# Kernel optimization log

Measured on AMD Instinct MI355X. Metric: run time of the kernel, lower is better.

Reference implementation:

```python
import jax, jax.numpy as jnp
import numpy as np

DISCOUNT = 0.997
LAMBDA = 0.95
LOSS_SCALE = 0.5
NUM_BINS = 255
BIN_LO, BIN_HI = -20.0, 20.0


def setup_inputs() -> dict:
    key = jax.random.key(0)
    k0, k1, k2, k3 = jax.random.split(key, 4)
    B, H, D = 1024, 16, 4096
    latents = jax.random.normal(k0, (B, H, D), dtype=jnp.float32)
    rewards = jax.random.normal(k1, (B, H), dtype=jnp.float32)
    dones = jnp.zeros((B, H), dtype=jnp.float32)
    bootstrap_latent = jax.random.normal(k2, (B, D), dtype=jnp.float32)
    W = jax.random.normal(k3, (D, NUM_BINS), dtype=jnp.float32) * (1.0 / np.sqrt(D))
    b = jnp.zeros((NUM_BINS,), dtype=jnp.float32)
    return {"latents": latents, "rewards": rewards, "dones": dones,
            "bootstrap_latent": bootstrap_latent, "W": W, "b": b}


def _bin_centers():
    return jnp.linspace(BIN_LO, BIN_HI, NUM_BINS, dtype=jnp.float32)


def _value_head(x, W, b):
    # x: (N, D) -> logits (N, K), value (N,)
    logits = x @ W + b
    value = jax.nn.softmax(logits, axis=-1) @ _bin_centers()
    return value, logits


def _target_to_bins(returns_flat):
    # two-hot encoding onto uniform bins; returns (N, K) soft target
    step = (BIN_HI - BIN_LO) / (NUM_BINS - 1)
    pos = (jnp.clip(returns_flat, BIN_LO, BIN_HI) - BIN_LO) / step  # in [0, K-1]
    low = jnp.clip(jnp.floor(pos).astype(jnp.int32), 0, NUM_BINS - 2)
    frac = pos - low.astype(pos.dtype)
    oh_lo = jax.nn.one_hot(low, NUM_BINS, dtype=returns_flat.dtype)
    oh_hi = jax.nn.one_hot(low + 1, NUM_BINS, dtype=returns_flat.dtype)
    return (1.0 - frac)[:, None] * oh_lo + frac[:, None] * oh_hi


def _lambda_returns(rewards, values, dones, bootstrap_value):
    # backward linear recurrence: G_t = r_t + gamma*mask_t*((1-lam)*V_{t+1} + lam*G_{t+1})
    next_values = jnp.concatenate([values[:, 1:], bootstrap_value[:, None]], axis=1)
    xs = (rewards.T, next_values.T, (1.0 - dones).T)  # time-major (H, B)

    def step(carry, x):
        r, nv, m = x
        g = r + DISCOUNT * m * ((1.0 - LAMBDA) * nv + LAMBDA * carry)
        return g, g

    _, outs = jax.lax.scan(step, bootstrap_value, xs, reverse=True)
    return outs.T  # (B, H)


def reference(latents, rewards, dones, bootstrap_latent, W, b):
    B, H = rewards.shape
    flat_latents = latents.reshape(-1, latents.shape[-1])  # (B*H, D)
    values_flat, logits = _value_head(flat_latents, W, b)
    values = values_flat.reshape(B, H)

    bootstrap_value, _ = _value_head(bootstrap_latent, W, b)
    bootstrap_value = jax.lax.stop_gradient(bootstrap_value)

    returns = jax.lax.stop_gradient(
        _lambda_returns(rewards, jax.lax.stop_gradient(values), dones, bootstrap_value))

    target = _target_to_bins(returns.reshape(-1))  # (B*H, K)
    logp = jax.nn.log_softmax(logits, axis=-1)
    value_loss = jnp.mean(-jnp.sum(target * logp, axis=-1))
    total_loss = LOSS_SCALE * value_loss

    return jnp.stack([total_loss, value_loss, values.mean(), returns.mean(),
                      jnp.std(values, ddof=1), jnp.std(returns, ddof=1)])
```

## Files before the change

kernel.cpp:

```cpp
#include <hip/hip_runtime.h>
#include <math.h>

#define NBINS 255
#define BIN_LO_F (-20.0f)
#define BIN_HI_F (20.0f)

typedef __attribute__((ext_vector_type(8))) short short8;
typedef __attribute__((ext_vector_type(16))) float f32x16;

__device__ __forceinline__ unsigned short f2bf(float f) {
    unsigned u = __builtin_bit_cast(unsigned, f);
    unsigned r = u + 0x7fffu + ((u >> 16) & 1u);
    return (unsigned short)(r >> 16);
}

__device__ __forceinline__ unsigned pkbf(float lo, float hi) {
    unsigned d;
    asm("v_cvt_pk_bf16_f32 %0, %1, %2" : "=v"(d) : "v"(lo), "v"(hi));
    return d;
}

__device__ __forceinline__ short8 mk8(unsigned a, unsigned b, unsigned c, unsigned d) {
    union { unsigned u[4]; short8 s; } t;
    t.u[0] = a; t.u[1] = b; t.u[2] = c; t.u[3] = d;
    return t.s;
}

__device__ __forceinline__ void glds16(const void* g, void* l) {
    __builtin_amdgcn_global_load_lds(
        (const __attribute__((address_space(1))) unsigned int*)g,
        (__attribute__((address_space(3))) unsigned int*)l, 16, 0, 0);
}

__device__ __forceinline__ double wave_reduce_sum_d(double v) {
    #pragma unroll
    for (int m = 32; m >= 1; m >>= 1) v += __shfl_xor(v, m, 64);
    return v;
}

__global__ __launch_bounds__(256) void pack_w4(
    const float* __restrict__ W, char* __restrict__ WpackB)
{
    int u = blockIdx.x * 256 + threadIdx.x;
    int kt = u >> 10;
    int v  = u & 1023;
    int ks = v >> 9;
    int lh = (v >> 8) & 1;
    int gcol = (v >> 5) & 7;
    int c31  = v & 31;
    int col  = gcol * 32 + c31;
    int k0   = kt * 32 + ks * 16 + lh * 8;
    short8 s;
    #pragma unroll
    for (int e = 0; e < 8; ++e)
        s[e] = (col < NBINS) ? (short)f2bf(W[(size_t)(k0 + e) * NBINS + col]) : (short)0;
    *(short8*)(WpackB + (size_t)u * 16) = s;
}

__global__ __launch_bounds__(256, 4) void gemm_mfma_v9(
    const float* __restrict__ latents, const float* __restrict__ boot,
    const char* __restrict__ WpackB, const float* __restrict__ bvec,
    float* __restrict__ logits, int NR, int R, int D, int nwg8)
{
    __shared__ __align__(16) char ldsA[2][4096];
    __shared__ __align__(16) char ldsB[2][16384];

    const int tid  = threadIdx.x;
    const int wave = tid >> 6, lane = tid & 63;
    const int l31  = lane & 31, lhi = lane >> 5;
    const int NT   = D >> 5;

    int bid  = blockIdx.x;
    int work = (bid & 7) * nwg8 + (bid >> 3);
    const int row0 = work * 32;

    const int arow_loc = (wave << 3) + (lane >> 3);
    const int arow = row0 + arow_loc;
    const float* arowp = (arow < NR) ? latents + (size_t)arow * D
                                     : boot + (size_t)(arow - NR) * D;
    const float* asrc = arowp + (((lane & 7) ^ (arow_loc & 7)) << 2);

    const int abase = l31 << 7;
    const int axor  = l31 & 7;

    f32x16 acc0, acc1;
    #pragma unroll
    for (int r = 0; r < 16; ++r) { acc0[r] = 0.f; acc1[r] = 0.f; }

#define STAGE(T, BUF) do {                                                  \
        glds16(asrc + (size_t)(T) * 32, &ldsA[BUF][(wave << 10) + (lane << 4)]); \
        const char* bs_ = WpackB + (size_t)(T) * 16384 + (wave << 12) + (lane << 4); \
        char* bd_ = &ldsB[BUF][(wave << 12) + (lane << 4)];                 \
        glds16(bs_,        bd_);                                            \
        glds16(bs_ + 1024, bd_ + 1024);                                     \
        glds16(bs_ + 2048, bd_ + 2048);                                     \
        glds16(bs_ + 3072, bd_ + 3072);                                     \
    } while (0)

#define COMPUTE(BUF) do {                                                   \
        const char* ab_ = &ldsA[BUF][0];                                    \
        const char* bb_ = &ldsB[BUF][0] + (wave << 10) + (l31 << 4);        \
        _Pragma("unroll")                                                   \
        for (int ks = 0; ks < 2; ++ks) {                                    \
            int c0_ = ks * 4 + lhi * 2;                                     \
            float4 f0_ = *(const float4*)(ab_ + abase + (((c0_ + 0) ^ axor) << 4)); \
            float4 f1_ = *(const float4*)(ab_ + abase + (((c0_ + 1) ^ axor) << 4)); \
            short8 a_  = mk8(pkbf(f0_.x, f0_.y), pkbf(f0_.z, f0_.w),        \
                             pkbf(f1_.x, f1_.y), pkbf(f1_.z, f1_.w));       \
            short8 b0_ = *(const short8*)(bb_ + ((ks * 2 + lhi) << 12));    \
            short8 b1_ = *(const short8*)(bb_ + ((ks * 2 + lhi) << 12) + 512); \
            acc0 = __builtin_amdgcn_mfma_f32_32x32x16_bf16(a_, b0_, acc0, 0, 0, 0); \
            acc1 = __builtin_amdgcn_mfma_f32_32x32x16_bf16(a_, b1_, acc1, 0, 0, 0); \
        }                                                                   \
    } while (0)

#define BAR()   __builtin_amdgcn_s_barrier()
#define SCHED() __builtin_amdgcn_sched_barrier(0)
#define WAITV5() asm volatile("s_waitcnt vmcnt(5)" ::: "memory")
#define WAITV0() asm volatile("s_waitcnt vmcnt(0)" ::: "memory")

    STAGE(0, 0);

    int t = 0;
    for (; t + 3 < NT; t += 2) {
        BAR(); SCHED(); STAGE(t + 1, 1); SCHED(); WAITV5(); BAR(); SCHED(); COMPUTE(0);
        BAR(); SCHED(); STAGE(t + 2, 0); SCHED(); WAITV5(); BAR(); SCHED(); COMPUTE(1);
    }
    BAR(); SCHED(); STAGE(NT - 1, 1); SCHED(); WAITV5(); BAR(); SCHED(); COMPUTE(0);
    BAR(); SCHED(); WAITV0(); BAR(); SCHED(); COMPUTE(1);

#undef STAGE
#undef COMPUTE
#undef BAR
#undef SCHED
#undef WAITV5
#undef WAITV0

    #pragma unroll
    for (int i = 0; i < 2; ++i) {
        int col = wave * 64 + i * 32 + l31;
        if (col < NBINS) {
            float bias = bvec[col];
            const f32x16& a = i ? acc1 : acc0;
            #pragma unroll
            for (int r = 0; r < 16; ++r) {
                int row = row0 + (r & 3) + 8 * (r >> 2) + 4 * lhi;
                logits[(size_t)row * NBINS + col] = a[r] + bias;
            }
        }
    }
}

__global__ __launch_bounds__(256) void softmax_stats(
    const float* __restrict__ logits, float* __restrict__ values,
    float* __restrict__ logZ, int R)
{
    int row  = blockIdx.x * 4 + (threadIdx.x >> 6);
    int lane = threadIdx.x & 63;
    if (row >= R) return;
    const float* lp = logits + (size_t)row * NBINS;
    const float step = (float)(40.0 / 254.0);

    float l[4];
    float m = -INFINITY;
    #pragma unroll
    for (int u = 0; u < 4; ++u) {
        int idx = lane + 64 * u;
        l[u] = (idx < NBINS) ? lp[idx] : -INFINITY;
        m = fmaxf(m, l[u]);
    }
    #pragma unroll
    for (int sh = 32; sh >= 1; sh >>= 1) m = fmaxf(m, __shfl_xor(m, sh, 64));

    float s = 0.f, sc = 0.f;
    #pragma unroll
    for (int u = 0; u < 4; ++u) {
        int idx = lane + 64 * u;
        if (idx < NBINS) {
            float e = __expf(l[u] - m);
            s  += e;
            sc += e * (BIN_LO_F + step * (float)idx);
        }
    }
    #pragma unroll
    for (int sh = 32; sh >= 1; sh >>= 1) {
        s  += __shfl_xor(s, sh, 64);
        sc += __shfl_xor(sc, sh, 64);
    }
    if (lane == 0) {
        values[row] = sc / s;
        logZ[row]   = m + __logf(s);
    }
}

__global__ void lambda_returns_k(
    const float* __restrict__ rewards, const float* __restrict__ dones,
    const float* __restrict__ values, float* __restrict__ returns,
    int B, int H, int NR)
{
    int b = blockIdx.x * blockDim.x + threadIdx.x;
    if (b >= B) return;
    const float gamma = 0.997f;
    const float lam   = 0.95f;
    const float oml   = (float)(1.0 - 0.95);
    float bootv = values[NR + b];
    float g = bootv;
    for (int h = H - 1; h >= 0; --h) {
        float nv   = (h == H - 1) ? bootv : values[b * H + h + 1];
        float mask = 1.0f - dones[b * H + h];
        g = rewards[b * H + h] + gamma * mask * (oml * nv + lam * g);
        returns[b * H + h] = g;
    }
}

__global__ __launch_bounds__(256) void loss_moments(
    const float* __restrict__ logits, const float* __restrict__ logZ,
    const float* __restrict__ values, const float* __restrict__ returns,
    double* __restrict__ accum, int NR)
{
    int row = blockIdx.x * blockDim.x + threadIdx.x;
    double lsum = 0, vsum = 0, v2 = 0, rsum = 0, r2 = 0;
    if (row < NR) {
        float v   = values[row];
        float ret = returns[row];
        float cl  = fminf(fmaxf(ret, BIN_LO_F), BIN_HI_F);
        const float step = (float)(40.0 / 254.0);
        float pos = (cl - BIN_LO_F) / step;
        int low = (int)floorf(pos);
        low = min(max(low, 0), NBINS - 2);
        float frac = pos - (float)low;
        const float* lp = logits + (size_t)row * NBINS;
        float llo = lp[low], lhi = lp[low + 1];
        float loss = logZ[row] - (1.f - frac) * llo - frac * lhi;
        lsum = (double)loss;
        vsum = (double)v;   v2 = (double)v * (double)v;
        rsum = (double)ret; r2 = (double)ret * (double)ret;
    }
    lsum = wave_reduce_sum_d(lsum);
    vsum = wave_reduce_sum_d(vsum);
    v2   = wave_reduce_sum_d(v2);
    rsum = wave_reduce_sum_d(rsum);
    r2   = wave_reduce_sum_d(r2);
    if ((threadIdx.x & 63) == 0) {
        atomicAdd(&accum[0], lsum);
        atomicAdd(&accum[1], vsum);
        atomicAdd(&accum[2], v2);
        atomicAdd(&accum[3], rsum);
        atomicAdd(&accum[4], r2);
    }
}

__global__ void finalize_k(const double* __restrict__ accum,
                           float* __restrict__ out, int NR)
{
    if (threadIdx.x == 0 && blockIdx.x == 0) {
        double n  = (double)NR;
        double vl = accum[0] / n;
        double mv = accum[1] / n;
        double vv = (accum[2] - n * mv * mv) / (n - 1.0);
        double mr = accum[3] / n;
        double vr = (accum[4] - n * mr * mr) / (n - 1.0);
        out[0] = (float)(0.5 * vl);
        out[1] = (float)vl;
        out[2] = (float)mv;
        out[3] = (float)mr;
        out[4] = (float)sqrt(vv > 0.0 ? vv : 0.0);
        out[5] = (float)sqrt(vr > 0.0 ? vr : 0.0);
    }
}

extern "C" void kernel_launch(void* const* d_in, const int* in_sizes, int n_in,
                              void* d_out, int out_size, void* d_ws, size_t ws_size,
                              hipStream_t stream) {
    const float* latents = (const float*)d_in[0];
    const float* rewards = (const float*)d_in[1];
    const float* dones   = (const float*)d_in[2];
    const float* boot    = (const float*)d_in[3];
    const float* W       = (const float*)d_in[4];
    const float* bvec    = (const float*)d_in[5];
    float* out = (float*)d_out;

    const int BH = in_sizes[1];
    const int D  = in_sizes[0] / BH;
    const int B  = in_sizes[3] / D;
    const int H  = BH / B;
    const int NR = BH;
    const int R  = NR + B;

    char* ws = (char*)d_ws;
    size_t off = 0;
    float* logits = (float*)(ws + off); off += (size_t)R * NBINS * sizeof(float);
    off = (off + 255) & ~(size_t)255;
    float* values = (float*)(ws + off); off += (size_t)R * sizeof(float);
    float* logZ   = (float*)(ws + off); off += (size_t)R * sizeof(float);
    float* rets   = (float*)(ws + off); off += (size_t)NR * sizeof(float);
    off = (off + 255) & ~(size_t)255;
    double* accum = (double*)(ws + off); off += 64;
    off = (off + 255) & ~(size_t)255;
    char* WpackB  = ws + off; off += (size_t)(D / 32) * 16384;

    hipMemsetAsync(accum, 0, 64, stream);

    const int NT = D / 32;
    const int packUnits = NT * 1024;
    pack_w4<<<packUnits / 256, 256, 0, stream>>>(W, WpackB);

    const int nwg = R / 32;
    gemm_mfma_v9<<<nwg, 256, 0, stream>>>(latents, boot, WpackB, bvec, logits,
                                          NR, R, D, nwg / 8);
    softmax_stats<<<(R + 3) / 4, 256, 0, stream>>>(logits, values, logZ, R);
    lambda_returns_k<<<(B + 255) / 256, 256, 0, stream>>>(rewards, dones, values, rets, B, H, NR);
    loss_moments<<<(NR + 255) / 256, 256, 0, stream>>>(logits, logZ, values, rets, accum, NR);
    finalize_k<<<1, 64, 0, stream>>>(accum, out, NR);
}
```

Measured before the change: 171.1 us.

## Split K in half with 64-row tiles and reduce partial logits downstream

The GEMM now splits the reduction dimension into two halves, giving 64x256 output tiles per workgroup with a 2x2 wave layout and four MFMAs per A fragment. Each half writes an unbiased partial-logit buffer (P0 or P1), and the softmax and loss kernels add the two partials plus the bias when they read. The aim is more MFMA work per staged tile and less per-block W traffic, at the same block count. The cost is twice the intermediate write and read traffic, a dropped LDS swizzle on the A tile, and a hard-coded 68 in the block-to-work mapping that only fits this problem size.

```diff
diff --git a/kernel.cpp b/kernel.cpp
--- a/kernel.cpp
+++ b/kernel.cpp
@@ -38,18 +38,17 @@
     return v;
 }
 
-__global__ __launch_bounds__(256) void pack_w4(
+__global__ __launch_bounds__(256) void pack_w5(
     const float* __restrict__ W, char* __restrict__ WpackB)
 {
     int u = blockIdx.x * 256 + threadIdx.x;
-    int kt = u >> 10;
-    int v  = u & 1023;
-    int ks = v >> 9;
-    int lh = (v >> 8) & 1;
+    int kt = u >> 9;
+    int v  = u & 511;
+    int lh = v >> 8;
     int gcol = (v >> 5) & 7;
     int c31  = v & 31;
     int col  = gcol * 32 + c31;
-    int k0   = kt * 32 + ks * 16 + lh * 8;
+    int k0   = kt * 16 + lh * 8;
     short8 s;
     #pragma unroll
     for (int e = 0; e < 8; ++e)
@@ -57,108 +56,106 @@
     *(short8*)(WpackB + (size_t)u * 16) = s;
 }
 
-__global__ __launch_bounds__(256, 4) void gemm_mfma_v9(
+__global__ __launch_bounds__(256, 4) void gemm_mfma_v10(
     const float* __restrict__ latents, const float* __restrict__ boot,
-    const char* __restrict__ WpackB, const float* __restrict__ bvec,
-    float* __restrict__ logits, int NR, int R, int D, int nwg8)
+    const char* __restrict__ WpackB, float* __restrict__ P0, float* __restrict__ P1,
+    int NR, int R, int D, int nMt)
 {
     __shared__ __align__(16) char ldsA[2][4096];
-    __shared__ __align__(16) char ldsB[2][16384];
+    __shared__ __align__(16) char ldsB[2][8192];
 
     const int tid  = threadIdx.x;
     const int wave = tid >> 6, lane = tid & 63;
     const int l31  = lane & 31, lhi = lane >> 5;
-    const int NT   = D >> 5;
+    const int mw   = wave & 1, nw = wave >> 1;
+    const int KH   = D >> 1;
+    const int NT   = KH >> 4;
 
     int bid  = blockIdx.x;
-    int work = (bid & 7) * nwg8 + (bid >> 3);
-    const int row0 = work * 32;
-
-    const int arow_loc = (wave << 3) + (lane >> 3);
-    const int arow = row0 + arow_loc;
+    int work = (bid & 7) * 68 + (bid >> 3);
+    const int kh = (work >= nMt) ? 1 : 0;
+    const int mt = work - kh * nMt;
+    const int row0 = mt * 64;
+    float* __restrict__ P = kh ? P1 : P0;
+
+    int arow = row0 + lane; if (arow > R - 1) arow = R - 1;
     const float* arowp = (arow < NR) ? latents + (size_t)arow * D
                                      : boot + (size_t)(arow - NR) * D;
-    const float* asrc = arowp + (((lane & 7) ^ (arow_loc & 7)) << 2);
-
-    const int abase = l31 << 7;
-    const int axor  = l31 & 7;
-
-    f32x16 acc0, acc1;
-    #pragma unroll
-    for (int r = 0; r < 16; ++r) { acc0[r] = 0.f; acc1[r] = 0.f; }
+    const float* asrc = arowp + kh * KH + wave * 4;
+    const char*  bbase = WpackB + (size_t)kh * ((size_t)NT * 8192)
+                                + (wave << 11) + (lane << 4);
+
+    f32x16 acc[4];
+    #pragma unroll
+    for (int g = 0; g < 4; ++g)
+        #pragma unroll
+        for (int r = 0; r < 16; ++r) acc[g][r] = 0.f;
 
 #define STAGE(T, BUF) do {                                                  \
-        glds16(asrc + (size_t)(T) * 32, &ldsA[BUF][(wave << 10) + (lane << 4)]); \
-        const char* bs_ = WpackB + (size_t)(T) * 16384 + (wave << 12) + (lane << 4); \
-        char* bd_ = &ldsB[BUF][(wave << 12) + (lane << 4)];                 \
+        glds16(asrc + (size_t)(T) * 16, &ldsA[BUF][(wave << 10) + (lane << 4)]); \
+        const char* bs_ = bbase + (size_t)(T) * 8192;                       \
+        char* bd_ = &ldsB[BUF][(wave << 11) + (lane << 4)];                 \
         glds16(bs_,        bd_);                                            \
         glds16(bs_ + 1024, bd_ + 1024);                                     \
-        glds16(bs_ + 2048, bd_ + 2048);                                     \
-        glds16(bs_ + 3072, bd_ + 3072);                                     \
     } while (0)
 
 #define COMPUTE(BUF) do {                                                   \
-        const char* ab_ = &ldsA[BUF][0];                                    \
-        const char* bb_ = &ldsB[BUF][0] + (wave << 10) + (l31 << 4);        \
+        const char* ab_ = &ldsA[BUF][0] + (lhi << 11) + (mw << 9) + (l31 << 4); \
+        const char* bb_ = &ldsB[BUF][0] + (lhi << 12) + (nw << 11) + (l31 << 4); \
+        float4 f0_ = *(const float4*)(ab_);                                 \
+        float4 f1_ = *(const float4*)(ab_ + 1024);                          \
+        short8 a_ = mk8(pkbf(f0_.x, f0_.y), pkbf(f0_.z, f0_.w),             \
+                        pkbf(f1_.x, f1_.y), pkbf(f1_.z, f1_.w));            \
         _Pragma("unroll")                                                   \
-        for (int ks = 0; ks < 2; ++ks) {                                    \
-            int c0_ = ks * 4 + lhi * 2;                                     \
-            float4 f0_ = *(const float4*)(ab_ + abase + (((c0_ + 0) ^ axor) << 4)); \
-            float4 f1_ = *(const float4*)(ab_ + abase + (((c0_ + 1) ^ axor) << 4)); \
-            short8 a_  = mk8(pkbf(f0_.x, f0_.y), pkbf(f0_.z, f0_.w),        \
-                             pkbf(f1_.x, f1_.y), pkbf(f1_.z, f1_.w));       \
-            short8 b0_ = *(const short8*)(bb_ + ((ks * 2 + lhi) << 12));    \
-            short8 b1_ = *(const short8*)(bb_ + ((ks * 2 + lhi) << 12) + 512); \
-            acc0 = __builtin_amdgcn_mfma_f32_32x32x16_bf16(a_, b0_, acc0, 0, 0, 0); \
-            acc1 = __builtin_amdgcn_mfma_f32_32x32x16_bf16(a_, b1_, acc1, 0, 0, 0); \
+        for (int g = 0; g < 4; ++g) {                                       \
+            short8 b_ = *(const short8*)(bb_ + (g << 9));                   \
+            acc[g] = __builtin_amdgcn_mfma_f32_32x32x16_bf16(a_, b_, acc[g], 0, 0, 0); \
         }                                                                   \
     } while (0)
 
 #define BAR()   __builtin_amdgcn_s_barrier()
 #define SCHED() __builtin_amdgcn_sched_barrier(0)
-#define WAITV5() asm volatile("s_waitcnt vmcnt(5)" ::: "memory")
+#define WAITV3() asm volatile("s_waitcnt vmcnt(3)" ::: "memory")
 #define WAITV0() asm volatile("s_waitcnt vmcnt(0)" ::: "memory")
 
     STAGE(0, 0);
 
     int t = 0;
     for (; t + 3 < NT; t += 2) {
-        BAR(); SCHED(); STAGE(t + 1, 1); SCHED(); WAITV5(); BAR(); SCHED(); COMPUTE(0);
-        BAR(); SCHED(); STAGE(t + 2, 0); SCHED(); WAITV5(); BAR(); SCHED(); COMPUTE(1);
-    }
-    BAR(); SCHED(); STAGE(NT - 1, 1); SCHED(); WAITV5(); BAR(); SCHED(); COMPUTE(0);
+        BAR(); SCHED(); STAGE(t + 1, 1); SCHED(); WAITV3(); BAR(); SCHED(); COMPUTE(0);
+        BAR(); SCHED(); STAGE(t + 2, 0); SCHED(); WAITV3(); BAR(); SCHED(); COMPUTE(1);
+    }
+    BAR(); SCHED(); STAGE(NT - 1, 1); SCHED(); WAITV3(); BAR(); SCHED(); COMPUTE(0);
     BAR(); SCHED(); WAITV0(); BAR(); SCHED(); COMPUTE(1);
 
 #undef STAGE
 #undef COMPUTE
 #undef BAR
 #undef SCHED
-#undef WAITV5
+#undef WAITV3
 #undef WAITV0
 
     #pragma unroll
-    for (int i = 0; i < 2; ++i) {
-        int col = wave * 64 + i * 32 + l31;
-        if (col < NBINS) {
-            float bias = bvec[col];
-            const f32x16& a = i ? acc1 : acc0;
-            #pragma unroll
-            for (int r = 0; r < 16; ++r) {
-                int row = row0 + (r & 3) + 8 * (r >> 2) + 4 * lhi;
-                logits[(size_t)row * NBINS + col] = a[r] + bias;
-            }
+    for (int g = 0; g < 4; ++g) {
+        int col = nw * 128 + g * 32 + l31;
+        #pragma unroll
+        for (int r = 0; r < 16; ++r) {
+            int row = row0 + mw * 32 + (r & 3) + 8 * (r >> 2) + 4 * lhi;
+            P[(size_t)row * 256 + col] = acc[g][r];
         }
     }
 }
 
-__global__ __launch_bounds__(256) void softmax_stats(
-    const float* __restrict__ logits, float* __restrict__ values,
+__global__ __launch_bounds__(256) void softmax_stats2(
+    const float* __restrict__ P0, const float* __restrict__ P1,
+    const float* __restrict__ bvec, float* __restrict__ values,
     float* __restrict__ logZ, int R)
 {
     int row  = blockIdx.x * 4 + (threadIdx.x >> 6);
     int lane = threadIdx.x & 63;
     if (row >= R) return;
-    const float* lp = logits + (size_t)row * NBINS;
+    const float* p0 = P0 + (size_t)row * 256;
+    const float* p1 = P1 + (size_t)row * 256;
     const float step = (float)(40.0 / 254.0);
 
     float l[4];
@@ -166,7 +163,7 @@
     #pragma unroll
     for (int u = 0; u < 4; ++u) {
         int idx = lane + 64 * u;
-        l[u] = (idx < NBINS) ? lp[idx] : -INFINITY;
+        l[u] = (idx < NBINS) ? (p0[idx] + p1[idx] + bvec[idx]) : -INFINITY;
         m = fmaxf(m, l[u]);
     }
     #pragma unroll
@@ -213,8 +210,9 @@
     }
 }
 
-__global__ __launch_bounds__(256) void loss_moments(
-    const float* __restrict__ logits, const float* __restrict__ logZ,
+__global__ __launch_bounds__(256) void loss_moments2(
+    const float* __restrict__ P0, const float* __restrict__ P1,
+    const float* __restrict__ bvec, const float* __restrict__ logZ,
     const float* __restrict__ values, const float* __restrict__ returns,
     double* __restrict__ accum, int NR)
 {
@@ -229,8 +227,9 @@
         int low = (int)floorf(pos);
         low = min(max(low, 0), NBINS - 2);
         float frac = pos - (float)low;
-        const float* lp = logits + (size_t)row * NBINS;
-        float llo = lp[low], lhi = lp[low + 1];
+        size_t base = (size_t)row * 256;
+        float llo = P0[base + low]     + P1[base + low]     + bvec[low];
+        float lhi = P0[base + low + 1] + P1[base + low + 1] + bvec[low + 1];
         float loss = logZ[row] - (1.f - frac) * llo - frac * lhi;
         lsum = (double)loss;
         vsum = (double)v;   v2 = (double)v * (double)v;
@@ -289,27 +288,27 @@
 
     char* ws = (char*)d_ws;
     size_t off = 0;
-    float* logits = (float*)(ws + off); off += (size_t)R * NBINS * sizeof(float);
-    off = (off + 255) & ~(size_t)255;
+    float* P0 = (float*)(ws + off); off += (size_t)R * 256 * sizeof(float);
+    float* P1 = (float*)(ws + off); off += (size_t)R * 256 * sizeof(float);
     float* values = (float*)(ws + off); off += (size_t)R * sizeof(float);
     float* logZ   = (float*)(ws + off); off += (size_t)R * sizeof(float);
     float* rets   = (float*)(ws + off); off += (size_t)NR * sizeof(float);
     off = (off + 255) & ~(size_t)255;
     double* accum = (double*)(ws + off); off += 64;
     off = (off + 255) & ~(size_t)255;
-    char* WpackB  = ws + off; off += (size_t)(D / 32) * 16384;
+    char* WpackB  = ws + off; off += (size_t)(D / 16) * 8192;
 
     hipMemsetAsync(accum, 0, 64, stream);
 
-    const int NT = D / 32;
-    const int packUnits = NT * 1024;
-    pack_w4<<<packUnits / 256, 256, 0, stream>>>(W, WpackB);
-
-    const int nwg = R / 32;
-    gemm_mfma_v9<<<nwg, 256, 0, stream>>>(latents, boot, WpackB, bvec, logits,
-                                          NR, R, D, nwg / 8);
-    softmax_stats<<<(R + 3) / 4, 256, 0, stream>>>(logits, values, logZ, R);
+    const int packUnits = (D / 16) * 512;
+    pack_w5<<<packUnits / 256, 256, 0, stream>>>(W, WpackB);
+
+    const int nMt = R / 64;
+    const int nwg = nMt * 2;
+    gemm_mfma_v10<<<nwg, 256, 0, stream>>>(latents, boot, WpackB, P0, P1,
+                                           NR, R, D, nMt);
+    softmax_stats2<<<(R + 3) / 4, 256, 0, stream>>>(P0, P1, bvec, values, logZ, R);
     lambda_returns_k<<<(B + 255) / 256, 256, 0, stream>>>(rewards, dones, values, rets, B, H, NR);
-    loss_moments<<<(NR + 255) / 256, 256, 0, stream>>>(logits, logZ, values, rets, accum, NR);
+    loss_moments2<<<(NR + 255) / 256, 256, 0, stream>>>(P0, P1, bvec, logZ, values, rets, accum, NR);
     finalize_k<<<1, 64, 0, stream>>>(accum, out, NR);
 }
```

Result: slower. 191.0 us (+11.6%).
